# Kernel tuning notes

Measured on AMD Instinct MI355X. Metric: run time of the kernel, lower is better.

Reference implementation:

```python
import jax, jax.numpy as jnp
import numpy as np

B, C, Hh, Ww = 64, 128, 28, 28   # batch, channels, subband H, subband W (H/2, W/2 of input)
NB, BS = 4, 32                    # num_blocks, block_size (C = NB*BS)
ORI = 6                           # DTCWT orientation subbands


def setup_inputs() -> dict:
    key = jax.random.key(0)
    ks = jax.random.split(key, 7)
    return {
        "xl": jax.random.normal(ks[0], (B, C, Hh, Ww), jnp.float32),
        "xh": jax.random.normal(ks[1], (B, C, ORI, Hh, Ww, 2), jnp.float32),
        "w_ll": jax.random.normal(ks[2], (C, Hh, Ww), jnp.float32) * 0.02,
        "w1": jax.random.normal(ks[3], (2, NB, BS, BS), jnp.float32) * 0.02,
        "w2": jax.random.normal(ks[4], (2, NB, BS, BS), jnp.float32) * 0.02,
        "b1": jax.random.normal(ks[5], (2, NB, BS), jnp.float32) * 0.02,
        "b2": jax.random.normal(ks[6], (2, NB, BS), jnp.float32) * 0.02,
    }


def _mul(x, w):
    # block-diagonal matmul: x [..., nb, bs_in], w [nb, bs_in, bs_out]
    return jnp.einsum('...bd,bdk->...bk', x, w)


def reference(xl, xh, w_ll, w1, w2, b1, b2):
    # lowpass: elementwise weighting (broadcast over batch)
    xl_out = xl * w_ll

    b, c = xh.shape[0], xh.shape[1]
    # (B,C,6,H,W,2) -> (2,B,6,H,W,C) -> (2,B,6,H,W,NB,BS)
    x = jnp.transpose(xh, (5, 0, 2, 3, 4, 1))
    x = x.reshape(2, b, ORI, xh.shape[3], xh.shape[4], NB, BS)
    xr, xi = x[0], x[1]

    # complex block-diagonal layer 1 + ReLU
    r1 = jax.nn.relu(_mul(xr, w1[0]) - _mul(xi, w1[1]) + b1[0])
    i1 = jax.nn.relu(_mul(xr, w1[1]) + _mul(xi, w1[0]) + b1[1])
    # complex block-diagonal layer 2 (linear)
    r2 = _mul(r1, w2[0]) - _mul(i1, w2[1]) + b2[0]
    i2 = _mul(r1, w2[1]) + _mul(i1, w2[0]) + b2[1]

    # stack real/imag last, merge blocks back to C, restore (B,C,6,H,W,2)
    out = jnp.stack([r2, i2], axis=-1)                               # (B,6,H,W,NB,BS,2)
    out = out.reshape(b, ORI, xh.shape[3], xh.shape[4], NB * BS, 2)  # (B,6,H,W,C,2)
    xh_out = jnp.transpose(out, (0, 4, 1, 2, 3, 5))                  # (B,C,6,H,W,2)
    # softshrink lambd == 0.0 -> identity (the torch code skips it)
    return xl_out, xh_out
```

## Files before the change

kernel.cpp:

```cpp
#include <hip/hip_runtime.h>

typedef __bf16 bf16x8 __attribute__((ext_vector_type(8)));
typedef float  f32x4  __attribute__((ext_vector_type(4)));


static __device__ __forceinline__ unsigned short bf16bits(float f) {
  __bf16 h = (__bf16)f; return __builtin_bit_cast(unsigned short, h);
}
static __device__ __forceinline__ unsigned int pack2(float a, float b) {
  return (unsigned int)bf16bits(a) | ((unsigned int)bf16bits(b) << 16);
}

__global__ void prep_weights(const float* __restrict__ w1, const float* __restrict__ w2,
                             unsigned short* __restrict__ wg) {
  const int e = blockIdx.x * 256 + threadIdx.x;
  const int nb    = e >> 13;
  const int layer = (e >> 12) & 1;
  const int n = (e >> 6) & 63;
  const int k = e & 63;
  const float* w = layer ? w2 : w1;
  const int kk = k & 31, nn = n & 31;
  float v;
  if (n < 32) {
    v = (k < 32) ?  w[((0 * 4 + nb) * 32 + kk) * 32 + nn]
                 : -w[((1 * 4 + nb) * 32 + kk) * 32 + nn];
  } else {
    v = (k < 32) ?  w[((1 * 4 + nb) * 32 + kk) * 32 + nn]
                 :  w[((0 * 4 + nb) * 32 + kk) * 32 + nn];
  }
  const int pos = nb * 8192 + layer * 4096 + n * 64 + (((k >> 3) ^ ((n >> 1) & 7)) * 8) + (k & 7);
  wg[pos] = bf16bits(v);
}

__global__ __launch_bounds__(256, 4)
void fused_kernel(const float* __restrict__ xh, const unsigned short* __restrict__ wg,
                  const float* __restrict__ b1, const float* __restrict__ b2,
                  const float* __restrict__ xl, const float* __restrict__ wll,
                  float* __restrict__ out) {
  __shared__ __align__(16) unsigned short Xs[128 * 64];
  __shared__ __align__(16) unsigned short Ws[2 * 64 * 64];
  __shared__ __align__(16) float Bs[128];

  const int t = threadIdx.x;
  const int bi = blockIdx.x;

  if (bi >= 9408) {
    const int llb = bi - 9408;
    const float4* xi4 = reinterpret_cast<const float4*>(xl);
    const float4* w4  = reinterpret_cast<const float4*>(wll);
    float4* o4 = reinterpret_cast<float4*>(out);
#pragma unroll
    for (int j = 0; j < 4; ++j) {
      const int i = llb * 1024 + j * 256 + t;
      const float4 x = xi4[i];
      const float4 w = w4[i % 25088];
      float4 r; r.x = x.x * w.x; r.y = x.y * w.y; r.z = x.z * w.z; r.w = x.w * w.w;
      o4[i] = r;
    }
    return;
  }

  const int mt  = bi % 392;
  const int snb = bi / 392;
  const int ori = snb >> 2;
  const int nb  = snb & 3;
  const int p0 = mt << 7;

  char* XB = reinterpret_cast<char*>(Xs);
  const char* WB = reinterpret_cast<const char*>(Ws);
  const float* xb = xh + (size_t)(nb * 32) * 9408 + ori * 1568;
  float* ob = out + 6422528 + (size_t)(nb * 32) * 9408 + ori * 1568;

  f32x4 R[8];
  const int pp = t & 63;
  const int cb = (t >> 6) * 8;
  {
    const int P = p0 + 2 * pp;
    const int bb = P / 784;
    const int hw = P - bb * 784;
    const float* s = xb + (size_t)bb * 1204224 + (size_t)cb * 9408 + hw * 2;
#pragma unroll
    for (int j = 0; j < 8; ++j)
      R[j] = *reinterpret_cast<const f32x4*>(s + (size_t)j * 9408);
  }
  uint4 Wr[4];
  float Bv = 0.f;
  {
    const uint4* src = reinterpret_cast<const uint4*>(wg + nb * 8192);
#pragma unroll
    for (int it = 0; it < 4; ++it) Wr[it] = src[it * 256 + t];
  }
  if (t < 128) {
    const int layer = t >> 6, n = t & 63;
    const float* bsrc = layer ? b2 : b1;
    Bv = bsrc[((n >> 5) * 4 + nb) * 32 + (n & 31)];
  }
  __builtin_amdgcn_sched_barrier(0);

  {
    uint4* dst = reinterpret_cast<uint4*>(Ws);
#pragma unroll
    for (int it = 0; it < 4; ++it) dst[it * 256 + t] = Wr[it];
  }
  if (t < 128) Bs[t] = Bv;
  {
    const int p = 2 * pp;
    const int s0 = pp & 7;
    const int gr = t >> 6;
    char* row0 = XB + p * 128;
    char* row1 = row0 + 128;
    uint4 u;
    u.x = pack2(R[0].x, R[1].x);  u.y = pack2(R[2].x, R[3].x);
    u.z = pack2(R[4].x, R[5].x);  u.w = pack2(R[6].x, R[7].x);
    *reinterpret_cast<uint4*>(row0 + ((gr ^ s0) * 16)) = u;
    u.x = pack2(R[0].y, R[1].y);  u.y = pack2(R[2].y, R[3].y);
    u.z = pack2(R[4].y, R[5].y);  u.w = pack2(R[6].y, R[7].y);
    *reinterpret_cast<uint4*>(row0 + (((gr + 4) ^ s0) * 16)) = u;
    u.x = pack2(R[0].z, R[1].z);  u.y = pack2(R[2].z, R[3].z);
    u.z = pack2(R[4].z, R[5].z);  u.w = pack2(R[6].z, R[7].z);
    *reinterpret_cast<uint4*>(row1 + ((gr ^ s0) * 16)) = u;
    u.x = pack2(R[0].w, R[1].w);  u.y = pack2(R[2].w, R[3].w);
    u.z = pack2(R[4].w, R[5].w);  u.w = pack2(R[6].w, R[7].w);
    *reinterpret_cast<uint4*>(row1 + (((gr + 4) ^ s0) * 16)) = u;
  }
  __syncthreads();

  const int lane = t & 63;
  const int wv = t >> 6;
  const int lr = lane & 15;
  const int lg = lane >> 4;

  f32x4 acc[4][2];
#pragma unroll
  for (int mi = 0; mi < 4; ++mi)
#pragma unroll
    for (int ni = 0; ni < 2; ++ni)
      acc[mi][ni] = (f32x4){0.f, 0.f, 0.f, 0.f};

#pragma unroll
  for (int ks = 0; ks < 2; ++ks) {
    bf16x8 wf[4], xf[2];
#pragma unroll
    for (int mi = 0; mi < 4; ++mi) {
      const int n = mi * 16 + lr;
      wf[mi] = *reinterpret_cast<const bf16x8*>(WB + n * 128 + (((ks * 4 + lg) ^ ((n >> 1) & 7)) * 16));
    }
#pragma unroll
    for (int ni = 0; ni < 2; ++ni) {
      const int p = wv * 32 + ni * 16 + lr;
      xf[ni] = *reinterpret_cast<const bf16x8*>(XB + p * 128 + (((ks * 4 + lg) ^ ((p >> 1) & 7)) * 16));
    }
#pragma unroll
    for (int mi = 0; mi < 4; ++mi)
#pragma unroll
      for (int ni = 0; ni < 2; ++ni)
        acc[mi][ni] = __builtin_amdgcn_mfma_f32_16x16x32_bf16(wf[mi], xf[ni], acc[mi][ni], 0, 0, 0);
  }

#pragma unroll
  for (int mi = 0; mi < 4; ++mi) {
    const f32x4 bv = *reinterpret_cast<const f32x4*>(&Bs[mi * 16 + lg * 4]);
    const int gH = mi * 2 + (lg >> 1);
    const int offH = (lg & 1) * 8;
#pragma unroll
    for (int ni = 0; ni < 2; ++ni) {
      const int p = wv * 32 + ni * 16 + lr;
      const float h0 = fmaxf(acc[mi][ni][0] + bv[0], 0.f);
      const float h1 = fmaxf(acc[mi][ni][1] + bv[1], 0.f);
      const float h2 = fmaxf(acc[mi][ni][2] + bv[2], 0.f);
      const float h3 = fmaxf(acc[mi][ni][3] + bv[3], 0.f);
      uint2 u; u.x = pack2(h0, h1); u.y = pack2(h2, h3);
      *reinterpret_cast<uint2*>(XB + p * 128 + ((gH ^ ((p >> 1) & 7)) * 16) + offH) = u;
    }
  }

  f32x4 acc2[4][2];
#pragma unroll
  for (int mi = 0; mi < 4; ++mi)
#pragma unroll
    for (int ni = 0; ni < 2; ++ni)
      acc2[mi][ni] = (f32x4){0.f, 0.f, 0.f, 0.f};

#pragma unroll
  for (int ks = 0; ks < 2; ++ks) {
    bf16x8 wf[4], hf[2];
#pragma unroll
    for (int mi = 0; mi < 4; ++mi) {
      const int n = mi * 16 + lr;
      wf[mi] = *reinterpret_cast<const bf16x8*>(WB + 8192 + n * 128 + (((ks * 4 + lg) ^ ((n >> 1) & 7)) * 16));
    }
#pragma unroll
    for (int ni = 0; ni < 2; ++ni) {
      const int p = wv * 32 + ni * 16 + lr;
      hf[ni] = *reinterpret_cast<const bf16x8*>(XB + p * 128 + (((ks * 4 + lg) ^ ((p >> 1) & 7)) * 16));
    }
#pragma unroll
    for (int mi = 0; mi < 4; ++mi)
#pragma unroll
      for (int ni = 0; ni < 2; ++ni)
        acc2[mi][ni] = __builtin_amdgcn_mfma_f32_16x16x32_bf16(wf[mi], hf[ni], acc2[mi][ni], 0, 0, 0);
  }

#pragma unroll
  for (int ni = 0; ni < 2; ++ni) {
    const int p = wv * 32 + ni * 16 + lr;
    const int P = p0 + p;
    const int bb = P / 784;
    const int hw = P - bb * 784;
    float* obase = ob + (size_t)bb * 1204224 + hw * 2;
#pragma unroll
    for (int mi = 0; mi < 2; ++mi) {
      const f32x4 bre = *reinterpret_cast<const f32x4*>(&Bs[64 + mi * 16 + lg * 4]);
      const f32x4 bim = *reinterpret_cast<const f32x4*>(&Bs[64 + (mi + 2) * 16 + lg * 4]);
#pragma unroll
      for (int j = 0; j < 4; ++j) {
        const int c = mi * 16 + lg * 4 + j;
        float2 v;
        v.x = acc2[mi][ni][j] + bre[j];
        v.y = acc2[mi + 2][ni][j] + bim[j];
        *reinterpret_cast<float2*>(obase + (size_t)c * 9408) = v;
      }
    }
  }
}

extern "C" void kernel_launch(void* const* d_in, const int* in_sizes, int n_in,
                              void* d_out, int out_size, void* d_ws, size_t ws_size,
                              hipStream_t stream) {
  (void)in_sizes; (void)n_in; (void)out_size; (void)ws_size;
  const float* xl  = (const float*)d_in[0];
  const float* xh  = (const float*)d_in[1];
  const float* wll = (const float*)d_in[2];
  const float* w1  = (const float*)d_in[3];
  const float* w2  = (const float*)d_in[4];
  const float* b1  = (const float*)d_in[5];
  const float* b2  = (const float*)d_in[6];
  float* out = (float*)d_out;
  unsigned short* wg = (unsigned short*)d_ws;

  prep_weights<<<128, 256, 0, stream>>>(w1, w2, wg);
  fused_kernel<<<10976, 256, 0, stream>>>(xh, wg, b1, b2, xl, wll, out);
}
```

Measured before the change: 143.5 us.

## Process two pixel tiles per workgroup with register prefetch and XCD-aware block remap

Each workgroup now handles two 128-pixel tiles instead of one, so the weight and bias staging into LDS is amortized over twice the work. The global loads for the second tile are issued right after the first tile's data is packed into LDS, overlapping them with the first tile's MFMA work. Each wave now packs only its own 32 rows, so the rows a wave reads are the rows it wrote and no workgroup barrier is needed between tiles. Block indices are also remapped across the 8 XCDs so consecutive tiles of the same subband/block go to the same XCD. The cost is a smaller grid, which leaves fewer independent workgroups to hide latency, and more live registers.

```diff
diff --git a/kernel.cpp b/kernel.cpp
--- a/kernel.cpp
+++ b/kernel.cpp
@@ -44,8 +44,8 @@
   const int t = threadIdx.x;
   const int bi = blockIdx.x;
 
-  if (bi >= 9408) {
-    const int llb = bi - 9408;
+  if (bi >= 4704) {
+    const int llb = bi - 4704;
     const float4* xi4 = reinterpret_cast<const float4*>(xl);
     const float4* w4  = reinterpret_cast<const float4*>(wll);
     float4* o4 = reinterpret_cast<float4*>(out);
@@ -60,11 +60,18 @@
     return;
   }
 
-  const int mt  = bi % 392;
-  const int snb = bi / 392;
+  const int wgid = (bi & 7) * 588 + (bi >> 3);
+  const int mtg = wgid % 196;
+  const int snb = wgid / 196;
   const int ori = snb >> 2;
   const int nb  = snb & 3;
-  const int p0 = mt << 7;
+  const int p00 = mtg << 8;
+
+  const int lane = t & 63;
+  const int wv = t >> 6;
+  const int lr = lane & 15;
+  const int lg = lane >> 4;
+  const int m  = lane & 15;
 
   char* XB = reinterpret_cast<char*>(Xs);
   const char* WB = reinterpret_cast<const char*>(Ws);
@@ -72,17 +79,37 @@
   float* ob = out + 6422528 + (size_t)(nb * 32) * 9408 + ori * 1568;
 
   f32x4 R[8];
-  const int pp = t & 63;
-  const int cb = (t >> 6) * 8;
-  {
-    const int P = p0 + 2 * pp;
+
+  auto issueX = [&](int tb) {
+    const int P = tb + wv * 32 + 2 * m;
     const int bb = P / 784;
     const int hw = P - bb * 784;
-    const float* s = xb + (size_t)bb * 1204224 + (size_t)cb * 9408 + hw * 2;
+    const float* s = xb + (size_t)bb * 1204224 + (size_t)(lg * 8) * 9408 + hw * 2;
 #pragma unroll
     for (int j = 0; j < 8; ++j)
       R[j] = *reinterpret_cast<const f32x4*>(s + (size_t)j * 9408);
-  }
+  };
+  auto packX = [&]() {
+    const int row = wv * 32 + 2 * m;
+    const int s0 = (row >> 1) & 7;
+    char* row0 = XB + row * 128;
+    char* row1 = row0 + 128;
+    uint4 u;
+    u.x = pack2(R[0].x, R[1].x);  u.y = pack2(R[2].x, R[3].x);
+    u.z = pack2(R[4].x, R[5].x);  u.w = pack2(R[6].x, R[7].x);
+    *reinterpret_cast<uint4*>(row0 + ((lg ^ s0) * 16)) = u;
+    u.x = pack2(R[0].y, R[1].y);  u.y = pack2(R[2].y, R[3].y);
+    u.z = pack2(R[4].y, R[5].y);  u.w = pack2(R[6].y, R[7].y);
+    *reinterpret_cast<uint4*>(row0 + (((lg + 4) ^ s0) * 16)) = u;
+    u.x = pack2(R[0].z, R[1].z);  u.y = pack2(R[2].z, R[3].z);
+    u.z = pack2(R[4].z, R[5].z);  u.w = pack2(R[6].z, R[7].z);
+    *reinterpret_cast<uint4*>(row1 + ((lg ^ s0) * 16)) = u;
+    u.x = pack2(R[0].w, R[1].w);  u.y = pack2(R[2].w, R[3].w);
+    u.z = pack2(R[4].w, R[5].w);  u.w = pack2(R[6].w, R[7].w);
+    *reinterpret_cast<uint4*>(row1 + (((lg + 4) ^ s0) * 16)) = u;
+  };
+
+  issueX(p00);
   uint4 Wr[4];
   float Bv = 0.f;
   {
@@ -96,129 +123,112 @@
     Bv = bsrc[((n >> 5) * 4 + nb) * 32 + (n & 31)];
   }
   __builtin_amdgcn_sched_barrier(0);
-
   {
     uint4* dst = reinterpret_cast<uint4*>(Ws);
 #pragma unroll
     for (int it = 0; it < 4; ++it) dst[it * 256 + t] = Wr[it];
   }
   if (t < 128) Bs[t] = Bv;
-  {
-    const int p = 2 * pp;
-    const int s0 = pp & 7;
-    const int gr = t >> 6;
-    char* row0 = XB + p * 128;
-    char* row1 = row0 + 128;
-    uint4 u;
-    u.x = pack2(R[0].x, R[1].x);  u.y = pack2(R[2].x, R[3].x);
-    u.z = pack2(R[4].x, R[5].x);  u.w = pack2(R[6].x, R[7].x);
-    *reinterpret_cast<uint4*>(row0 + ((gr ^ s0) * 16)) = u;
-    u.x = pack2(R[0].y, R[1].y);  u.y = pack2(R[2].y, R[3].y);
-    u.z = pack2(R[4].y, R[5].y);  u.w = pack2(R[6].y, R[7].y);
-    *reinterpret_cast<uint4*>(row0 + (((gr + 4) ^ s0) * 16)) = u;
-    u.x = pack2(R[0].z, R[1].z);  u.y = pack2(R[2].z, R[3].z);
-    u.z = pack2(R[4].z, R[5].z);  u.w = pack2(R[6].z, R[7].z);
-    *reinterpret_cast<uint4*>(row1 + ((gr ^ s0) * 16)) = u;
-    u.x = pack2(R[0].w, R[1].w);  u.y = pack2(R[2].w, R[3].w);
-    u.z = pack2(R[4].w, R[5].w);  u.w = pack2(R[6].w, R[7].w);
-    *reinterpret_cast<uint4*>(row1 + (((gr + 4) ^ s0) * 16)) = u;
-  }
   __syncthreads();
 
-  const int lane = t & 63;
-  const int wv = t >> 6;
-  const int lr = lane & 15;
-  const int lg = lane >> 4;
-
-  f32x4 acc[4][2];
-#pragma unroll
-  for (int mi = 0; mi < 4; ++mi)
-#pragma unroll
-    for (int ni = 0; ni < 2; ++ni)
-      acc[mi][ni] = (f32x4){0.f, 0.f, 0.f, 0.f};
-
-#pragma unroll
-  for (int ks = 0; ks < 2; ++ks) {
-    bf16x8 wf[4], xf[2];
+#pragma unroll
+  for (int tt = 0; tt < 2; ++tt) {
+    const int p0t = p00 + tt * 128;
+
+    packX();
+    if (tt == 0) issueX(p00 + 128);
+    __builtin_amdgcn_sched_barrier(0);
+
+    f32x4 acc[4][2];
+#pragma unroll
+    for (int mi = 0; mi < 4; ++mi)
+#pragma unroll
+      for (int ni = 0; ni < 2; ++ni)
+        acc[mi][ni] = (f32x4){0.f, 0.f, 0.f, 0.f};
+
+#pragma unroll
+    for (int ks = 0; ks < 2; ++ks) {
+      bf16x8 wf[4], xf[2];
+#pragma unroll
+      for (int mi = 0; mi < 4; ++mi) {
+        const int n = mi * 16 + lr;
+        wf[mi] = *reinterpret_cast<const bf16x8*>(WB + n * 128 + (((ks * 4 + lg) ^ ((n >> 1) & 7)) * 16));
+      }
+#pragma unroll
+      for (int ni = 0; ni < 2; ++ni) {
+        const int p = wv * 32 + ni * 16 + lr;
+        xf[ni] = *reinterpret_cast<const bf16x8*>(XB + p * 128 + (((ks * 4 + lg) ^ ((p >> 1) & 7)) * 16));
+      }
+#pragma unroll
+      for (int mi = 0; mi < 4; ++mi)
+#pragma unroll
+        for (int ni = 0; ni < 2; ++ni)
+          acc[mi][ni] = __builtin_amdgcn_mfma_f32_16x16x32_bf16(wf[mi], xf[ni], acc[mi][ni], 0, 0, 0);
+    }
+
 #pragma unroll
     for (int mi = 0; mi < 4; ++mi) {
-      const int n = mi * 16 + lr;
-      wf[mi] = *reinterpret_cast<const bf16x8*>(WB + n * 128 + (((ks * 4 + lg) ^ ((n >> 1) & 7)) * 16));
-    }
+      const f32x4 bv = *reinterpret_cast<const f32x4*>(&Bs[mi * 16 + lg * 4]);
+      const int gH = mi * 2 + (lg >> 1);
+      const int offH = (lg & 1) * 8;
+#pragma unroll
+      for (int ni = 0; ni < 2; ++ni) {
+        const int p = wv * 32 + ni * 16 + lr;
+        const float h0 = fmaxf(acc[mi][ni][0] + bv[0], 0.f);
+        const float h1 = fmaxf(acc[mi][ni][1] + bv[1], 0.f);
+        const float h2 = fmaxf(acc[mi][ni][2] + bv[2], 0.f);
+        const float h3 = fmaxf(acc[mi][ni][3] + bv[3], 0.f);
+        uint2 u; u.x = pack2(h0, h1); u.y = pack2(h2, h3);
+        *reinterpret_cast<uint2*>(XB + p * 128 + ((gH ^ ((p >> 1) & 7)) * 16) + offH) = u;
+      }
+    }
+
+    f32x4 acc2[4][2];
+#pragma unroll
+    for (int mi = 0; mi < 4; ++mi)
+#pragma unroll
+      for (int ni = 0; ni < 2; ++ni)
+        acc2[mi][ni] = (f32x4){0.f, 0.f, 0.f, 0.f};
+
+#pragma unroll
+    for (int ks = 0; ks < 2; ++ks) {
+      bf16x8 wf[4], hf[2];
+#pragma unroll
+      for (int mi = 0; mi < 4; ++mi) {
+        const int n = mi * 16 + lr;
+        wf[mi] = *reinterpret_cast<const bf16x8*>(WB + 8192 + n * 128 + (((ks * 4 + lg) ^ ((n >> 1) & 7)) * 16));
+      }
+#pragma unroll
+      for (int ni = 0; ni < 2; ++ni) {
+        const int p = wv * 32 + ni * 16 + lr;
+        hf[ni] = *reinterpret_cast<const bf16x8*>(XB + p * 128 + (((ks * 4 + lg) ^ ((p >> 1) & 7)) * 16));
+      }
+#pragma unroll
+      for (int mi = 0; mi < 4; ++mi)
+#pragma unroll
+        for (int ni = 0; ni < 2; ++ni)
+          acc2[mi][ni] = __builtin_amdgcn_mfma_f32_16x16x32_bf16(wf[mi], hf[ni], acc2[mi][ni], 0, 0, 0);
+    }
+
 #pragma unroll
     for (int ni = 0; ni < 2; ++ni) {
       const int p = wv * 32 + ni * 16 + lr;
-      xf[ni] = *reinterpret_cast<const bf16x8*>(XB + p * 128 + (((ks * 4 + lg) ^ ((p >> 1) & 7)) * 16));
-    }
-#pragma unroll
-    for (int mi = 0; mi < 4; ++mi)
-#pragma unroll
-      for (int ni = 0; ni < 2; ++ni)
-        acc[mi][ni] = __builtin_amdgcn_mfma_f32_16x16x32_bf16(wf[mi], xf[ni], acc[mi][ni], 0, 0, 0);
-  }
-
-#pragma unroll
-  for (int mi = 0; mi < 4; ++mi) {
-    const f32x4 bv = *reinterpret_cast<const f32x4*>(&Bs[mi * 16 + lg * 4]);
-    const int gH = mi * 2 + (lg >> 1);
-    const int offH = (lg & 1) * 8;
-#pragma unroll
-    for (int ni = 0; ni < 2; ++ni) {
-      const int p = wv * 32 + ni * 16 + lr;
-      const float h0 = fmaxf(acc[mi][ni][0] + bv[0], 0.f);
-      const float h1 = fmaxf(acc[mi][ni][1] + bv[1], 0.f);
-      const float h2 = fmaxf(acc[mi][ni][2] + bv[2], 0.f);
-      const float h3 = fmaxf(acc[mi][ni][3] + bv[3], 0.f);
-      uint2 u; u.x = pack2(h0, h1); u.y = pack2(h2, h3);
-      *reinterpret_cast<uint2*>(XB + p * 128 + ((gH ^ ((p >> 1) & 7)) * 16) + offH) = u;
-    }
-  }
-
-  f32x4 acc2[4][2];
-#pragma unroll
-  for (int mi = 0; mi < 4; ++mi)
-#pragma unroll
-    for (int ni = 0; ni < 2; ++ni)
-      acc2[mi][ni] = (f32x4){0.f, 0.f, 0.f, 0.f};
-
-#pragma unroll
-  for (int ks = 0; ks < 2; ++ks) {
-    bf16x8 wf[4], hf[2];
-#pragma unroll
-    for (int mi = 0; mi < 4; ++mi) {
-      const int n = mi * 16 + lr;
-      wf[mi] = *reinterpret_cast<const bf16x8*>(WB + 8192 + n * 128 + (((ks * 4 + lg) ^ ((n >> 1) & 7)) * 16));
-    }
-#pragma unroll
-    for (int ni = 0; ni < 2; ++ni) {
-      const int p = wv * 32 + ni * 16 + lr;
-      hf[ni] = *reinterpret_cast<const bf16x8*>(XB + p * 128 + (((ks * 4 + lg) ^ ((p >> 1) & 7)) * 16));
-    }
-#pragma unroll
-    for (int mi = 0; mi < 4; ++mi)
-#pragma unroll
-      for (int ni = 0; ni < 2; ++ni)
-        acc2[mi][ni] = __builtin_amdgcn_mfma_f32_16x16x32_bf16(wf[mi], hf[ni], acc2[mi][ni], 0, 0, 0);
-  }
-
-#pragma unroll
-  for (int ni = 0; ni < 2; ++ni) {
-    const int p = wv * 32 + ni * 16 + lr;
-    const int P = p0 + p;
-    const int bb = P / 784;
-    const int hw = P - bb * 784;
-    float* obase = ob + (size_t)bb * 1204224 + hw * 2;
-#pragma unroll
-    for (int mi = 0; mi < 2; ++mi) {
-      const f32x4 bre = *reinterpret_cast<const f32x4*>(&Bs[64 + mi * 16 + lg * 4]);
-      const f32x4 bim = *reinterpret_cast<const f32x4*>(&Bs[64 + (mi + 2) * 16 + lg * 4]);
-#pragma unroll
-      for (int j = 0; j < 4; ++j) {
-        const int c = mi * 16 + lg * 4 + j;
-        float2 v;
-        v.x = acc2[mi][ni][j] + bre[j];
-        v.y = acc2[mi + 2][ni][j] + bim[j];
-        *reinterpret_cast<float2*>(obase + (size_t)c * 9408) = v;
+      const int P = p0t + p;
+      const int bb = P / 784;
+      const int hw = P - bb * 784;
+      float* obase = ob + (size_t)bb * 1204224 + hw * 2;
+#pragma unroll
+      for (int mi = 0; mi < 2; ++mi) {
+        const f32x4 bre = *reinterpret_cast<const f32x4*>(&Bs[64 + mi * 16 + lg * 4]);
+        const f32x4 bim = *reinterpret_cast<const f32x4*>(&Bs[64 + (mi + 2) * 16 + lg * 4]);
+#pragma unroll
+        for (int j = 0; j < 4; ++j) {
+          const int c = mi * 16 + lg * 4 + j;
+          float2 v;
+          v.x = acc2[mi][ni][j] + bre[j];
+          v.y = acc2[mi + 2][ni][j] + bim[j];
+          *reinterpret_cast<float2*>(obase + (size_t)c * 9408) = v;
+        }
       }
     }
   }
@@ -239,5 +249,5 @@
   unsigned short* wg = (unsigned short*)d_ws;
 
   prep_weights<<<128, 256, 0, stream>>>(w1, w2, wg);
-  fused_kernel<<<10976, 256, 0, stream>>>(xh, wg, b1, b2, xl, wll, out);
-}
+  fused_kernel<<<6272, 256, 0, stream>>>(xh, wg, b1, b2, xl, wll, out);
+}
```

Result: no change. 142.4 us (-0.8%).
